# Optimization experiments

Hardware: AMD Instinct MI355X
Metric: run time of the kernel (lower is better)

Reference implementation:

```python
import jax, jax.numpy as jnp
import numpy as np

IMG_SIZE = 256
NUM_ANGLES = 180
NUM_DETECTORS = 363
BATCH = 4


def setup_inputs() -> dict:
    key = jax.random.key(0)
    sinogram = jax.random.normal(key, (BATCH, 1, NUM_ANGLES, NUM_DETECTORS), dtype=jnp.float32)
    return {"sinogram": sinogram}


def _fbp(sinogram):
    B, C, A, D = sinogram.shape
    # --- ramp filter in frequency domain (filter_type='ramp') ---
    freq = jnp.fft.fftfreq(D).astype(jnp.float32)
    filt = jnp.abs(freq) * 2.0
    sino_fft = jnp.fft.fft(sinogram, axis=-1)
    filtered = jnp.fft.ifft(sino_fft * filt, axis=-1).real.astype(jnp.float32)  # (B,1,A,D)

    # --- backprojection (adjoint Radon), vectorized over all angles ---
    coords = jnp.linspace(-1.0, 1.0, IMG_SIZE, dtype=jnp.float32)
    y_grid, x_grid = jnp.meshgrid(coords, coords, indexing='ij')  # (H,W)
    angles = jnp.linspace(0.0, np.pi, A, dtype=jnp.float32)       # torch.linspace includes endpoint
    cos_t = jnp.cos(angles)[:, None, None]
    sin_t = jnp.sin(angles)[:, None, None]
    t = x_grid[None] * cos_t + y_grid[None] * sin_t               # (A,H,W), in [-sqrt2, sqrt2]

    # grid_sample bilinear, align_corners=True, padding_mode='zeros' along detector axis
    px = (t + 1.0) * 0.5 * (D - 1)                                # pixel coordinate
    i0 = jnp.floor(px).astype(jnp.int32)
    frac = px - i0.astype(jnp.float32)
    i1 = i0 + 1
    m0 = ((i0 >= 0) & (i0 <= D - 1)).astype(jnp.float32)
    m1 = ((i1 >= 0) & (i1 <= D - 1)).astype(jnp.float32)
    i0c = jnp.clip(i0, 0, D - 1).reshape(A, -1)                   # (A,N) N=H*W
    i1c = jnp.clip(i1, 0, D - 1).reshape(A, -1)
    w0 = ((1.0 - frac) * m0).reshape(A, -1)
    w1 = (frac * m1).reshape(A, -1)

    sino2 = filtered[:, 0]                                        # (B,A,D)
    a_idx = jnp.arange(A)[:, None]
    g0 = sino2[:, a_idx, i0c]                                     # (B,A,N)
    g1 = sino2[:, a_idx, i1c]
    recon = (g0 * w0 + g1 * w1).sum(axis=1)                       # (B,N)
    recon = recon * (np.pi / A)
    return recon.reshape(B, C, IMG_SIZE, IMG_SIZE)


def reference(sinogram):
    return _fbp(sinogram)
```

## Files before the change

kernel.cpp:

```cpp
#include <hip/hip_runtime.h>
#include <math.h>

#define D_   363
#define A_   180
#define B_   4
#define IMG_ 256

__global__ __launch_bounds__(512)
void fbp_prep(float* __restrict__ h,
              float* __restrict__ ctab,
              float* __restrict__ stab) {
    __shared__ float red[512];
    const int n = blockIdx.x;
    const int k = threadIdx.x;

    float term = 0.0f;
    if (k < D_) {
        int mk = (k < D_ - k) ? k : (D_ - k);
        float filt = (2.0f * (float)mk) / (float)D_;
        int p = (k * n) % D_;
        float ang = (float)(2.0 * M_PI) * ((float)p / (float)D_);
        term = filt * cosf(ang);
    }
    red[k] = term;
    __syncthreads();
    #pragma unroll
    for (int s = 256; s > 0; s >>= 1) {
        if (k < s) red[k] += red[k + s];
        __syncthreads();
    }
    if (k == 0) h[n] = red[0] / (float)D_;

    if (n == 0 && k < A_) {
        double a = (double)k * (M_PI / 179.0);
        ctab[k] = (float)cos(a);
        stab[k] = (float)sin(a);
    }
}

__global__ __launch_bounds__(384)
void fbp_filter(const float* __restrict__ sino,
                const float* __restrict__ h,
                float* __restrict__ filtered) {
    __shared__ float4 hext4[2 * D_];
    const int r   = blockIdx.x;
    const int tid = threadIdx.x;

    for (int j = tid; j < 2 * D_; j += 384) {
        float a = h[ j              % D_];
        float b = h[(j - 1 + D_)    % D_];
        float c = h[(j - 2 + D_)    % D_];
        float d = h[(j - 3 + D_)    % D_];
        hext4[j] = make_float4(a, b, c, d);
    }
    __syncthreads();

    if (tid < D_) {
        const float* srow_g = sino + r * D_;
        float acc = 0.0f;
        int base = tid + D_;
        #pragma unroll 5
        for (int m = 0; m < 360; m += 4) {
            float s0 = srow_g[m];
            float s1 = srow_g[m + 1];
            float s2 = srow_g[m + 2];
            float s3 = srow_g[m + 3];
            float4 hv = hext4[base - m];
            acc = fmaf(s0, hv.x, acc);
            acc = fmaf(s1, hv.y, acc);
            acc = fmaf(s2, hv.z, acc);
            acc = fmaf(s3, hv.w, acc);
        }
        {
            float4 hv = hext4[base - 360];
            acc = fmaf(srow_g[360], hv.x, acc);
            acc = fmaf(srow_g[361], hv.y, acc);
            acc = fmaf(srow_g[362], hv.z, acc);
        }
        filtered[r * D_ + tid] = acc;
    }
}

__global__ __launch_bounds__(256)
void fbp_backproj(const float* __restrict__ filtered,
                  const float* __restrict__ ctab,
                  const float* __restrict__ stab,
                  float* __restrict__ out) {
    __shared__ float cl[A_], sl[A_];
    const int tid = threadIdx.x;
    if (tid < A_) { cl[tid] = ctab[tid]; sl[tid] = stab[tid]; }
    __syncthreads();

    const int tile = blockIdx.x & 255;
    const int b    = blockIdx.x >> 8;
    const int ty   = tid >> 4, tx = tid & 15;
    const int i = ((tile >> 4) << 4) + ty;
    const int j = ((tile & 15) << 4) + tx;

    const float y = -1.0f + 2.0f * (float)i / 255.0f;
    const float x = -1.0f + 2.0f * (float)j / 255.0f;

    const float* fb = filtered + b * (A_ * D_);
    float acc = 0.0f;

    for (int a = 0; a < A_; ++a) {
        float t  = x * cl[a] + y * sl[a];
        float px = (t + 1.0f) * 0.5f * 362.0f;
        float fi = floorf(px);
        float frac = px - fi;
        int i0 = (int)fi;
        int i1 = i0 + 1;
        float w0 = (i0 >= 0 && i0 <= D_ - 1) ? (1.0f - frac) : 0.0f;
        float w1 = (i1 >= 0 && i1 <= D_ - 1) ? frac          : 0.0f;
        int i0c = min(max(i0, 0), D_ - 1);
        int i1c = min(max(i1, 0), D_ - 1);
        const float* row = fb + a * D_;
        acc = fmaf(row[i0c], w0, acc);
        acc = fmaf(row[i1c], w1, acc);
    }
    out[(b << 16) + i * IMG_ + j] = acc * (float)(M_PI / 180.0);
}

extern "C" void kernel_launch(void* const* d_in, const int* in_sizes, int n_in,
                              void* d_out, int out_size, void* d_ws, size_t ws_size,
                              hipStream_t stream) {
    const float* sino = (const float*)d_in[0];
    float* out = (float*)d_out;
    float* ws  = (float*)d_ws;

    float* h        = ws;
    float* ctab     = ws + 384;
    float* stab     = ws + 576;
    float* filtered = ws + 768;

    fbp_prep    <<<D_,       512, 0, stream>>>(h, ctab, stab);
    fbp_filter  <<<B_ * A_,  384, 0, stream>>>(sino, h, filtered);
    fbp_backproj<<<B_ * IMG_, 256, 0, stream>>>(filtered, ctab, stab, out);
}
```

Before: 96.24 us.

## Eliminate prep kernel using closed-form ramp filter and inline trig tables

Removes the separate prep launch by computing the circular ramp-filter impulse response in closed form inside the filter kernel, and by computing the cos/sin tables inline in the backprojection kernel. The filter kernel also stages the sinogram row in shared memory and reads it as float4. The backprojection folds the coordinate scale into the tables so each angle needs fewer ops, and it unrolls the angle loop. This saves one launch and the global round trips for the tables, at the cost of some redundant trig per block and possible small float differences from the closed-form filter.

```diff
diff --git a/kernel.cpp b/kernel.cpp
--- a/kernel.cpp
+++ b/kernel.cpp
@@ -6,76 +6,53 @@
 #define B_   4
 #define IMG_ 256
 
-__global__ __launch_bounds__(512)
-void fbp_prep(float* __restrict__ h,
-              float* __restrict__ ctab,
-              float* __restrict__ stab) {
-    __shared__ float red[512];
-    const int n = blockIdx.x;
-    const int k = threadIdx.x;
-
-    float term = 0.0f;
-    if (k < D_) {
-        int mk = (k < D_ - k) ? k : (D_ - k);
-        float filt = (2.0f * (float)mk) / (float)D_;
-        int p = (k * n) % D_;
-        float ang = (float)(2.0 * M_PI) * ((float)p / (float)D_);
-        term = filt * cosf(ang);
-    }
-    red[k] = term;
-    __syncthreads();
-    #pragma unroll
-    for (int s = 256; s > 0; s >>= 1) {
-        if (k < s) red[k] += red[k + s];
-        __syncthreads();
-    }
-    if (k == 0) h[n] = red[0] / (float)D_;
-
-    if (n == 0 && k < A_) {
-        double a = (double)k * (M_PI / 179.0);
-        ctab[k] = (float)cos(a);
-        stab[k] = (float)sin(a);
-    }
-}
-
 __global__ __launch_bounds__(384)
 void fbp_filter(const float* __restrict__ sino,
-                const float* __restrict__ h,
                 float* __restrict__ filtered) {
-    __shared__ float4 hext4[2 * D_];
+    __shared__ __align__(16) float  srow[364];
+    __shared__ float                hval[D_];
+    __shared__ __align__(16) float4 hext4[2 * D_];
     const int r   = blockIdx.x;
     const int tid = threadIdx.x;
 
+    if (tid < D_) {
+        srow[tid] = sino[r * D_ + tid];
+        float hn;
+        if (tid == 0) {
+            hn = 65884.0f / 131769.0f;
+        } else {
+            int p1 = (181 * tid) % D_;
+            int p2 = (182 * tid) % D_;
+            float c1 = cosf(6.28318530717958647692f * ((float)p1 * (1.0f / 363.0f)));
+            float c2 = cosf(6.28318530717958647692f * ((float)p2 * (1.0f / 363.0f)));
+            float sh = sinf(3.14159265358979323846f * ((float)tid * (1.0f / 363.0f)));
+            float S  = (182.0f * c1 - 181.0f * c2 - 1.0f) / (4.0f * sh * sh);
+            hn = S * (4.0f / 131769.0f);
+        }
+        hval[tid] = hn;
+    }
+    if (tid == D_) srow[D_] = 0.0f;
+    __syncthreads();
+
     for (int j = tid; j < 2 * D_; j += 384) {
-        float a = h[ j              % D_];
-        float b = h[(j - 1 + D_)    % D_];
-        float c = h[(j - 2 + D_)    % D_];
-        float d = h[(j - 3 + D_)    % D_];
+        float a = hval[ j            % D_];
+        float b = hval[(j + D_ - 1)  % D_];
+        float c = hval[(j + D_ - 2)  % D_];
+        float d = hval[(j + D_ - 3)  % D_];
         hext4[j] = make_float4(a, b, c, d);
     }
     __syncthreads();
 
     if (tid < D_) {
-        const float* srow_g = sino + r * D_;
         float acc = 0.0f;
-        int base = tid + D_;
-        #pragma unroll 5
-        for (int m = 0; m < 360; m += 4) {
-            float s0 = srow_g[m];
-            float s1 = srow_g[m + 1];
-            float s2 = srow_g[m + 2];
-            float s3 = srow_g[m + 3];
-            float4 hv = hext4[base - m];
-            acc = fmaf(s0, hv.x, acc);
-            acc = fmaf(s1, hv.y, acc);
-            acc = fmaf(s2, hv.z, acc);
-            acc = fmaf(s3, hv.w, acc);
-        }
-        {
-            float4 hv = hext4[base - 360];
-            acc = fmaf(srow_g[360], hv.x, acc);
-            acc = fmaf(srow_g[361], hv.y, acc);
-            acc = fmaf(srow_g[362], hv.z, acc);
+        #pragma unroll 7
+        for (int q = 0; q < 91; ++q) {
+            float4 sv = *(const float4*)&srow[4 * q];
+            float4 hv = hext4[tid + D_ - 4 * q];
+            acc = fmaf(sv.x, hv.x, acc);
+            acc = fmaf(sv.y, hv.y, acc);
+            acc = fmaf(sv.z, hv.z, acc);
+            acc = fmaf(sv.w, hv.w, acc);
         }
         filtered[r * D_ + tid] = acc;
     }
@@ -83,12 +60,16 @@
 
 __global__ __launch_bounds__(256)
 void fbp_backproj(const float* __restrict__ filtered,
-                  const float* __restrict__ ctab,
-                  const float* __restrict__ stab,
                   float* __restrict__ out) {
     __shared__ float cl[A_], sl[A_];
     const int tid = threadIdx.x;
-    if (tid < A_) { cl[tid] = ctab[tid]; sl[tid] = stab[tid]; }
+    if (tid < A_) {
+        float a = (float)((double)tid * (3.14159265358979323846 / 179.0));
+        float sn, cn;
+        sincosf(a, &sn, &cn);
+        cl[tid] = 181.0f * cn;
+        sl[tid] = 181.0f * sn;
+    }
     __syncthreads();
 
     const int tile = blockIdx.x & 255;
@@ -100,18 +81,18 @@
     const float y = -1.0f + 2.0f * (float)i / 255.0f;
     const float x = -1.0f + 2.0f * (float)j / 255.0f;
 
-    const float* fb = filtered + b * (A_ * D_);
+    const float* __restrict__ fb = filtered + b * (A_ * D_);
     float acc = 0.0f;
 
+    #pragma unroll 4
     for (int a = 0; a < A_; ++a) {
-        float t  = x * cl[a] + y * sl[a];
-        float px = (t + 1.0f) * 0.5f * 362.0f;
+        float px = fmaf(x, cl[a], fmaf(y, sl[a], 181.0f));
         float fi = floorf(px);
         float frac = px - fi;
         int i0 = (int)fi;
         int i1 = i0 + 1;
-        float w0 = (i0 >= 0 && i0 <= D_ - 1) ? (1.0f - frac) : 0.0f;
-        float w1 = (i1 >= 0 && i1 <= D_ - 1) ? frac          : 0.0f;
+        float w0 = ((unsigned)i0 <= (unsigned)(D_ - 1)) ? (1.0f - frac) : 0.0f;
+        float w1 = ((unsigned)i1 <= (unsigned)(D_ - 1)) ? frac          : 0.0f;
         int i0c = min(max(i0, 0), D_ - 1);
         int i1c = min(max(i1, 0), D_ - 1);
         const float* row = fb + a * D_;
@@ -126,14 +107,8 @@
                               hipStream_t stream) {
     const float* sino = (const float*)d_in[0];
     float* out = (float*)d_out;
-    float* ws  = (float*)d_ws;
+    float* filtered = (float*)d_ws;
 
-    float* h        = ws;
-    float* ctab     = ws + 384;
-    float* stab     = ws + 576;
-    float* filtered = ws + 768;
-
-    fbp_prep    <<<D_,       512, 0, stream>>>(h, ctab, stab);
-    fbp_filter  <<<B_ * A_,  384, 0, stream>>>(sino, h, filtered);
-    fbp_backproj<<<B_ * IMG_, 256, 0, stream>>>(filtered, ctab, stab, out);
+    fbp_filter  <<<B_ * A_,   384, 0, stream>>>(sino, filtered);
+    fbp_backproj<<<B_ * IMG_, 256, 0, stream>>>(filtered, out);
 }
```

After: 92.16 us. 4.2% less time.
